# Kernel optimization log

Hardware: AMD Instinct MI355X
Metric: run time of the kernel (lower is better)

Reference implementation:

```python
import jax, jax.numpy as jnp
import numpy as np

EMBED = 1024
HEADS = 16
DIM_HEAD = EMBED // HEADS
N, L = 4, 2048


def setup_inputs() -> dict:
    key = jax.random.key(0)
    ks = jax.random.split(key, 12)
    s = 0.02
    return {
        "q": jax.random.normal(ks[0], (N, L, EMBED), jnp.float32),
        "k": jax.random.normal(ks[1], (N, L, EMBED), jnp.float32),
        "v": jax.random.normal(ks[2], (N, L, EMBED), jnp.float32),
        "padding_mask": jnp.ones((N, L), dtype=bool),
        "sequence_mask": jnp.zeros((L, L), dtype=bool),
        # Linear(in, out): store weight as [out, in] like torch, bias [out]
        "Wq": jax.random.normal(ks[3], (EMBED, EMBED), jnp.float32) * s,
        "bq": jnp.zeros((EMBED,), jnp.float32),
        "Wk": jax.random.normal(ks[4], (EMBED, EMBED), jnp.float32) * s,
        "bk": jnp.zeros((EMBED,), jnp.float32),
        "Wv": jax.random.normal(ks[5], (EMBED, EMBED), jnp.float32) * s,
        "bv": jnp.zeros((EMBED,), jnp.float32),
        "Wo": jax.random.normal(ks[6], (EMBED, EMBED), jnp.float32) * s,
        "bo": jnp.zeros((EMBED,), jnp.float32),
    }


def reference(q, k, v, padding_mask, sequence_mask, Wq, bq, Wk, bk, Wv, bv, Wo, bo):
    n, lq, _ = q.shape
    lk = k.shape[1]
    # input projections
    qp = (q @ Wq.T + bq).reshape(n, lq, HEADS, DIM_HEAD)
    kp = (k @ Wk.T + bk).reshape(n, lk, HEADS, DIM_HEAD)
    vp = (v @ Wv.T + bv).reshape(n, lk, HEADS, DIM_HEAD)
    # energy: [n, h, lq, lk]
    energy = jnp.einsum('nqhd,nkhd->nhqk', qp, kp)
    attention = jax.nn.softmax(energy / jnp.sqrt(jnp.float32(EMBED)), axis=3)
    # NOTE: the original torch code calls masked_fill (non in-place) and
    # discards the result, so padding_mask / sequence_mask have NO effect.
    # Dropout is also never applied in forward. Replicated faithfully.
    out = jnp.einsum('nhqk,nkhd->nqhd', attention, vp)
    out = out.reshape(n, lq, EMBED)
    return out @ Wo.T + bo
```

## Files before the change

### kernel.cpp

```cpp
#include <hip/hip_runtime.h>
#include <stdint.h>

typedef _Float16 f16;
typedef _Float16 f16x8 __attribute__((ext_vector_type(8)));
typedef _Float16 f16x4 __attribute__((ext_vector_type(4)));
typedef _Float16 f16x2 __attribute__((ext_vector_type(2)));
typedef float f32x4 __attribute__((ext_vector_type(4)));

__device__ __forceinline__ f32x4 mfma16(f16x8 a, f16x8 b, f32x4 c) {
    return __builtin_amdgcn_mfma_f32_16x16x32_f16(a, b, c, 0, 0, 0);
}

__device__ __forceinline__ void gload16(const f16* g, f16* l) {
    __builtin_amdgcn_global_load_lds(
        (const __attribute__((address_space(1))) uint32_t*)g,
        (__attribute__((address_space(3))) uint32_t*)l, 16, 0, 0);
}

__device__ __forceinline__ f16x8 cvt8(f32x4 a, f32x4 b) {
    f16x8 h;
    h[0] = (f16)a[0]; h[1] = (f16)a[1]; h[2] = (f16)a[2]; h[3] = (f16)a[3];
    h[4] = (f16)b[0]; h[5] = (f16)b[1]; h[6] = (f16)b[2]; h[7] = (f16)b[3];
    return h;
}

template <bool A16, bool OUT16>
__device__ __forceinline__ void gemm_fused(const void* __restrict__ Av,
                                           const float* __restrict__ B,
                                           const float* __restrict__ bias,
                                           void* __restrict__ Cout, long ldo,
                                           int biasrow, float scale,
                                           long m0, long n0, f16* As, f16* Bs) {
    int tid = threadIdx.x;
    int lane = tid & 63, w = tid >> 6;
    int wm = w & 1, wn = w >> 1;
    int l15 = lane & 15, quad = lane >> 4;

    int r4 = lane >> 2;
    int g = lane & 3;
    int sc = g ^ ((r4 >> 1) & 3);
    int c4 = (lane & 3) ^ ((lane >> 3) & 3);

    const f16* a16 = (const f16*)Av;
    const float* a32 = (const float*)Av;

    const f16* a16src[2];
    const float* a32src[2];
    const float* b32src[2];
    int lwoff[2];
#pragma unroll
    for (int t = 0; t < 2; ++t) {
        long row = t * 64 + w * 16 + r4;
        if constexpr (A16)
            a16src[t] = a16 + (m0 + row) * 1024 + c4 * 8;
        else
            a32src[t] = a32 + (m0 + row) * 1024 + g * 8;
        b32src[t] = B + (n0 + row) * 1024 + g * 8;
        lwoff[t] = t * 2048 + w * 512;
    }
    int wroff = r4 * 32 + sc * 8;

    f32x4 acc[4][4] = {};

#pragma unroll
    for (int t = 0; t < 2; ++t) {
        if constexpr (A16) {
            gload16(a16src[t], As + lwoff[t]);
        } else {
            f32x4 x0 = *(const f32x4*)(a32src[t]);
            f32x4 x1 = *(const f32x4*)(a32src[t] + 4);
            *(f16x8*)&As[lwoff[t] + wroff] = cvt8(x0, x1);
        }
        f32x4 y0 = *(const f32x4*)(b32src[t]);
        f32x4 y1 = *(const f32x4*)(b32src[t] + 4);
        *(f16x8*)&Bs[lwoff[t] + wroff] = cvt8(y0, y1);
    }
    if constexpr (A16) asm volatile("s_waitcnt vmcnt(0)" ::: "memory");
    asm volatile("s_waitcnt lgkmcnt(0)" ::: "memory");
    __builtin_amdgcn_s_barrier();
    __builtin_amdgcn_sched_barrier(0);

    for (int kt = 0; kt < 32; ++kt) {
        int cur = kt & 1;
        int nxt = cur ^ 1;
        f32x4 la[2][2], lb[2][2];
        if (kt < 31) {
            long ko = (long)(kt + 1) * 32;
#pragma unroll
            for (int t = 0; t < 2; ++t) {
                if constexpr (A16) {
                    gload16(a16src[t] + ko, As + nxt * 4096 + lwoff[t]);
                } else {
                    la[t][0] = *(const f32x4*)(a32src[t] + ko);
                    la[t][1] = *(const f32x4*)(a32src[t] + ko + 4);
                }
                lb[t][0] = *(const f32x4*)(b32src[t] + ko);
                lb[t][1] = *(const f32x4*)(b32src[t] + ko + 4);
            }
        }
        const f16* as = As + cur * 4096;
        const f16* bs = Bs + cur * 4096;
        int cs = (quad ^ ((l15 >> 1) & 3)) * 8;
        f16x8 af[4], bf[4];
#pragma unroll
        for (int t = 0; t < 4; ++t) {
            af[t] = *(const f16x8*)&as[(wm * 64 + t * 16 + l15) * 32 + cs];
            bf[t] = *(const f16x8*)&bs[(wn * 64 + t * 16 + l15) * 32 + cs];
        }
        __builtin_amdgcn_s_setprio(1);
#pragma unroll
        for (int i = 0; i < 4; ++i)
#pragma unroll
            for (int j = 0; j < 4; ++j)
                acc[i][j] = mfma16(af[i], bf[j], acc[i][j]);
        __builtin_amdgcn_s_setprio(0);
        if (kt < 31) {
#pragma unroll
            for (int t = 0; t < 2; ++t) {
                if constexpr (!A16)
                    *(f16x8*)&As[nxt * 4096 + lwoff[t] + wroff] =
                        cvt8(la[t][0], la[t][1]);
                *(f16x8*)&Bs[nxt * 4096 + lwoff[t] + wroff] =
                    cvt8(lb[t][0], lb[t][1]);
            }
            if constexpr (A16) asm volatile("s_waitcnt vmcnt(0)" ::: "memory");
            asm volatile("s_waitcnt lgkmcnt(0)" ::: "memory");
            __builtin_amdgcn_s_barrier();
            __builtin_amdgcn_sched_barrier(0);
        }
    }

#pragma unroll
    for (int i = 0; i < 4; ++i) {
        int mrow = wm * 64 + i * 16 + quad * 4;
#pragma unroll
        for (int j = 0; j < 4; ++j) {
            int ncol = wn * 64 + j * 16 + l15;
            long gn = n0 + ncol;
#pragma unroll
            for (int r = 0; r < 4; ++r) {
                long gm = m0 + mrow + r;
                float v = (acc[i][j][r] + (biasrow ? bias[gm] : bias[gn])) * scale;
                if constexpr (OUT16)
                    ((f16*)Cout)[gm * ldo + gn] = (f16)v;
                else
                    ((float*)Cout)[gm * ldo + gn] = v;
            }
        }
    }
}

__global__ __launch_bounds__(256, 2) void qkv_proj(
    const float* __restrict__ q, const float* __restrict__ k,
    const float* __restrict__ v, const float* __restrict__ Wq,
    const float* __restrict__ Wk, const float* __restrict__ Wv,
    const float* __restrict__ bq, const float* __restrict__ bk,
    const float* __restrict__ bv, f16* __restrict__ Qp, f16* __restrict__ Kp,
    f16* __restrict__ Vt) {
    __shared__ __align__(16) f16 As[2 * 4096];
    __shared__ __align__(16) f16 Bs[2 * 4096];
    int z = blockIdx.z;
    const float* A;
    const float* B;
    const float* bias;
    f16* C;
    long ldo;
    int biasrow;
    float scale;
    if (z == 0) {
        A = q; B = Wq; bias = bq; C = Qp; ldo = 1024; biasrow = 0;
        scale = 0.0450842200277786f;
    } else if (z == 1) {
        A = k; B = Wk; bias = bk; C = Kp; ldo = 1024; biasrow = 0;
        scale = 1.0f;
    } else {
        A = Wv; B = v; bias = bv; C = Vt; ldo = 8192; biasrow = 1;
        scale = 1.0f;
    }
    long m0 = (long)(z == 2 ? blockIdx.y : blockIdx.x) * 128;
    long n0 = (long)(z == 2 ? blockIdx.x : blockIdx.y) * 128;
    gemm_fused<false, true>(A, B, bias, C, ldo, biasrow, scale, m0, n0, As, Bs);
}

__global__ __launch_bounds__(256, 2) void o_proj(const f16* __restrict__ Op,
                                                 const float* __restrict__ Wo,
                                                 const float* __restrict__ bo,
                                                 float* __restrict__ out) {
    __shared__ __align__(16) f16 As[2 * 4096];
    __shared__ __align__(16) f16 Bs[2 * 4096];
    gemm_fused<true, false>(Op, Wo, bo, out, 1024, 0, 1.0f,
                            (long)blockIdx.x * 128, (long)blockIdx.y * 128,
                            As, Bs);
}

__global__ __launch_bounds__(256, 2) void attn256(const f16* __restrict__ Qp,
                                                  const f16* __restrict__ Kp,
                                                  const f16* __restrict__ Vt,
                                                  f16* __restrict__ Op) {
    __shared__ __align__(16) f16 Ps0[128 * 64];
    __shared__ __align__(16) f16 Ps1[128 * 64];
    __shared__ __align__(16) f16 Ks[3][64 * 64];
    __shared__ __align__(16) f16 Vs[3][64 * 64];

    int tid = threadIdx.x;
    int lane = tid & 63, w = tid >> 6;
    int l15 = lane & 15, quad = lane >> 4;
    int b = blockIdx.x;
    int xcd = b & 7, slot = b >> 3;
    int nh = xcd * 8 + (slot >> 3);
    int qp = slot & 7;
    int nb = nh >> 4, h = nh & 15;
    long tok0 = (long)nb * 2048;
    long qrow0 = qp * 256;

    int rg = lane >> 3, cg = (lane & 7) ^ rg;

    const f16* qsrc0 = Qp + (tok0 + qrow0) * 1024 + h * 64;
    const f16* qsrc1 = qsrc0 + 128 * 1024;
#pragma unroll
    for (int t = 0; t < 4; ++t) {
        int rb = w * 32 + t * 8;
        gload16(qsrc0 + (rb + rg) * 1024 + cg * 8, &Ps0[rb * 64]);
        gload16(qsrc1 + (rb + rg) * 1024 + cg * 8, &Ps1[rb * 64]);
    }
    const f16* kptr = Kp + (tok0 + w * 16 + rg) * 1024 + h * 64 + cg * 8;
    const f16* vptr = Vt + ((long)h * 64 + w * 16 + rg) * 8192 + tok0 + cg * 8;
    gload16(kptr, &Ks[0][(w * 16) * 64]);
    gload16(kptr + 8 * 1024, &Ks[0][(w * 16 + 8) * 64]);
    gload16(vptr, &Vs[0][(w * 16) * 64]);
    gload16(vptr + (long)8 * 8192, &Vs[0][(w * 16 + 8) * 64]);
    gload16(kptr + 65536, &Ks[1][(w * 16) * 64]);
    gload16(kptr + 65536 + 8 * 1024, &Ks[1][(w * 16 + 8) * 64]);
    gload16(vptr + 64, &Vs[1][(w * 16) * 64]);
    gload16(vptr + 64 + (long)8 * 8192, &Vs[1][(w * 16 + 8) * 64]);
    const f16* kn = kptr + 2 * 65536;
    const f16* vn = vptr + 2 * 64;

    asm volatile("s_waitcnt vmcnt(8)" ::: "memory");
    f16x8 qf0[2][2], qf1[2][2];
#pragma unroll
    for (int ks = 0; ks < 2; ++ks) {
        int cc = (ks * 4 + quad) ^ (l15 & 7);
#pragma unroll
        for (int j = 0; j < 2; ++j) {
            qf0[ks][j] = *(const f16x8*)&Ps0[(w * 32 + j * 16 + l15) * 64 + cc * 8];
            qf1[ks][j] = *(const f16x8*)&Ps1[(w * 32 + j * 16 + l15) * 64 + cc * 8];
        }
    }
    asm volatile("s_waitcnt vmcnt(4)" ::: "memory");
    __builtin_amdgcn_s_barrier();
    __builtin_amdgcn_sched_barrier(0);

    f32x4 oacc0[2][4] = {}, oacc1[2][4] = {};
    float rs0[2] = {0.f, 0.f}, rs1[2] = {0.f, 0.f};
    const f32x4 z4 = {0.f, 0.f, 0.f, 0.f};

    int cur = 0;
    for (int kt = 0; kt < 32; ++kt) {
        f32x4 sacc0[4][2], sacc1[4][2];
        __builtin_amdgcn_s_setprio(1);
#pragma unroll
        for (int ks = 0; ks < 2; ++ks) {
            int cc = (ks * 4 + quad) ^ (l15 & 7);
            f16x8 a[4];
#pragma unroll
            for (int t = 0; t < 4; ++t)
                a[t] = *(const f16x8*)&Ks[cur][(t * 16 + l15) * 64 + cc * 8];
#pragma unroll
            for (int i = 0; i < 4; ++i)
#pragma unroll
                for (int j = 0; j < 2; ++j) {
                    if (ks == 0) {
                        sacc0[i][j] = mfma16(a[i], qf0[0][j], z4);
                        sacc1[i][j] = mfma16(a[i], qf1[0][j], z4);
                    } else {
                        sacc0[i][j] = mfma16(a[i], qf0[1][j], sacc0[i][j]);
                        sacc1[i][j] = mfma16(a[i], qf1[1][j], sacc1[i][j]);
                    }
                }
        }
        __builtin_amdgcn_s_setprio(0);
        if (kt < 30) {
            int nxt = (cur == 0) ? 2 : cur - 1;
            f16* kd = &Ks[nxt][(w * 16) * 64];
            f16* vd = &Vs[nxt][(w * 16) * 64];
            gload16(kn, kd);
            gload16(kn + 8 * 1024, kd + 8 * 64);
            gload16(vn, vd);
            gload16(vn + (long)8 * 8192, vd + 8 * 64);
            kn += 65536;
            vn += 64;
        }
#pragma unroll
        for (int i = 0; i < 4; ++i) {
#pragma unroll
            for (int j = 0; j < 2; ++j) {
                int qrow = w * 32 + j * 16 + l15;
                int kl = i * 16 + quad * 4;
                int c = kl >> 3;
                int off = qrow * 64 + ((c ^ (qrow & 7)) << 3) + (kl & 7);
                {
                    float p0 = __builtin_amdgcn_exp2f(sacc0[i][j][0]);
                    float p1 = __builtin_amdgcn_exp2f(sacc0[i][j][1]);
                    float p2 = __builtin_amdgcn_exp2f(sacc0[i][j][2]);
                    float p3 = __builtin_amdgcn_exp2f(sacc0[i][j][3]);
                    rs0[j] += (p0 + p1) + (p2 + p3);
                    f16x2 lo = __builtin_bit_cast(f16x2, __builtin_amdgcn_cvt_pkrtz(p0, p1));
                    f16x2 hi = __builtin_bit_cast(f16x2, __builtin_amdgcn_cvt_pkrtz(p2, p3));
                    f16x4 ph;
                    ph[0] = lo[0]; ph[1] = lo[1]; ph[2] = hi[0]; ph[3] = hi[1];
                    *(f16x4*)&Ps0[off] = ph;
                }
                {
                    float p0 = __builtin_amdgcn_exp2f(sacc1[i][j][0]);
                    float p1 = __builtin_amdgcn_exp2f(sacc1[i][j][1]);
                    float p2 = __builtin_amdgcn_exp2f(sacc1[i][j][2]);
                    float p3 = __builtin_amdgcn_exp2f(sacc1[i][j][3]);
                    rs1[j] += (p0 + p1) + (p2 + p3);
                    f16x2 lo = __builtin_bit_cast(f16x2, __builtin_amdgcn_cvt_pkrtz(p0, p1));
                    f16x2 hi = __builtin_bit_cast(f16x2, __builtin_amdgcn_cvt_pkrtz(p2, p3));
                    f16x4 ph;
                    ph[0] = lo[0]; ph[1] = lo[1]; ph[2] = hi[0]; ph[3] = hi[1];
                    *(f16x4*)&Ps1[off] = ph;
                }
            }
        }
        __builtin_amdgcn_s_setprio(1);
#pragma unroll
        for (int ks = 0; ks < 2; ++ks) {
            int cc = (ks * 4 + quad) ^ (l15 & 7);
            f16x8 bf[4];
#pragma unroll
            for (int j = 0; j < 4; ++j)
                bf[j] = *(const f16x8*)&Vs[cur][(j * 16 + l15) * 64 + cc * 8];
            f16x8 af0[2], af1[2];
#pragma unroll
            for (int i = 0; i < 2; ++i) {
                af0[i] = *(const f16x8*)&Ps0[(w * 32 + i * 16 + l15) * 64 + cc * 8];
                af1[i] = *(const f16x8*)&Ps1[(w * 32 + i * 16 + l15) * 64 + cc * 8];
            }
#pragma unroll
            for (int i = 0; i < 2; ++i)
#pragma unroll
                for (int j = 0; j < 4; ++j) {
                    oacc0[i][j] = mfma16(af0[i], bf[j], oacc0[i][j]);
                    oacc1[i][j] = mfma16(af1[i], bf[j], oacc1[i][j]);
                }
        }
        __builtin_amdgcn_s_setprio(0);
        if (kt < 31) {
            if (kt < 30)
                asm volatile("s_waitcnt vmcnt(4)" ::: "memory");
            else
                asm volatile("s_waitcnt vmcnt(0)" ::: "memory");
            __builtin_amdgcn_s_barrier();
            __builtin_amdgcn_sched_barrier(0);
        }
        cur = (cur == 2) ? 0 : cur + 1;
    }

    float* lsi = (float*)&Ks[0][0];
#pragma unroll
    for (int j = 0; j < 2; ++j) {
        rs0[j] += __shfl_xor(rs0[j], 16, 64);
        rs0[j] += __shfl_xor(rs0[j], 32, 64);
        rs1[j] += __shfl_xor(rs1[j], 16, 64);
        rs1[j] += __shfl_xor(rs1[j], 32, 64);
    }
    if (lane < 16) {
        lsi[w * 32 + lane] = 1.0f / rs0[0];
        lsi[w * 32 + 16 + lane] = 1.0f / rs0[1];
        lsi[128 + w * 32 + lane] = 1.0f / rs1[0];
        lsi[128 + w * 32 + 16 + lane] = 1.0f / rs1[1];
    }

    long otok = tok0 + qrow0;
#pragma unroll
    for (int i = 0; i < 2; ++i) {
        int qrow = w * 32 + i * 16 + quad * 4;
#pragma unroll
        for (int j = 0; j < 4; ++j) {
            int d = j * 16 + l15;
#pragma unroll
            for (int r = 0; r < 4; ++r) {
                Op[(otok + qrow + r) * 1024 + h * 64 + d] =
                    (f16)(oacc0[i][j][r] * lsi[qrow + r]);
                Op[(otok + 128 + qrow + r) * 1024 + h * 64 + d] =
                    (f16)(oacc1[i][j][r] * lsi[128 + qrow + r]);
            }
        }
    }
}

extern "C" void kernel_launch(void* const* d_in, const int* in_sizes, int n_in,
                              void* d_out, int out_size, void* d_ws, size_t ws_size,
                              hipStream_t stream) {
    const float* q  = (const float*)d_in[0];
    const float* k  = (const float*)d_in[1];
    const float* v  = (const float*)d_in[2];
    const float* Wq = (const float*)d_in[5];
    const float* bq = (const float*)d_in[6];
    const float* Wk = (const float*)d_in[7];
    const float* bk = (const float*)d_in[8];
    const float* Wv = (const float*)d_in[9];
    const float* bv = (const float*)d_in[10];
    const float* Wo = (const float*)d_in[11];
    const float* bo = (const float*)d_in[12];

    char* ws = (char*)d_ws;
    f16* Qp = (f16*)ws;
    f16* Kp = (f16*)(ws + (16L << 20));
    f16* Vt = (f16*)(ws + (32L << 20));
    f16* Op = (f16*)(ws + (48L << 20));

    qkv_proj<<<dim3(64, 8, 3), 256, 0, stream>>>(q, k, v, Wq, Wk, Wv,
                                                 bq, bk, bv, Qp, Kp, Vt);

    attn256<<<512, 256, 0, stream>>>(Qp, Kp, Vt, Op);

    o_proj<<<dim3(64, 8), 256, 0, stream>>>(Op, Wo, bo, (float*)d_out);
}
```

Baseline: 358.8 us.

## Deepen projection GEMM pipeline to three LDS stages with XCD-aware block mapping

Rewrites the shared projection GEMM as a three-stage LDS pipeline. The activation operand is prefetched into registers three k-tiles ahead, while the weight operand is staged one tile ahead. The async global_load_lds path for the fp16 A operand is replaced with register loads plus LDS stores. Block indices are remapped so that all blocks on one XCD share the same weight column tile, aiming for better L2 reuse. The costs are more LDS (48KB per block), higher register pressure from the in-flight prefetch buffers, and a possible loss of occupancy at two blocks per CU.

```diff
diff --git a/kernel.cpp b/kernel.cpp
--- a/kernel.cpp
+++ b/kernel.cpp
@@ -24,111 +24,142 @@
     return h;
 }
 
-template <bool A16, bool OUT16>
-__device__ __forceinline__ void gemm_fused(const void* __restrict__ Av,
-                                           const float* __restrict__ B,
-                                           const float* __restrict__ bias,
-                                           void* __restrict__ Cout, long ldo,
-                                           int biasrow, float scale,
-                                           long m0, long n0, f16* As, f16* Bs) {
+template <bool DEEP16, bool OUT16>
+__device__ __forceinline__ void gemm_fused(
+    const void* __restrict__ Dmat, const float* __restrict__ Smat,
+    long d0, long s0, bool deepA, const float* __restrict__ bias,
+    void* __restrict__ Cout, long ldo, int biasrow, float scale,
+    long m0, long n0, f16* As, f16* Bs) {
     int tid = threadIdx.x;
     int lane = tid & 63, w = tid >> 6;
     int wm = w & 1, wn = w >> 1;
     int l15 = lane & 15, quad = lane >> 4;
-
     int r4 = lane >> 2;
     int g = lane & 3;
     int sc = g ^ ((r4 >> 1) & 3);
-    int c4 = (lane & 3) ^ ((lane >> 3) & 3);
-
-    const f16* a16 = (const f16*)Av;
-    const float* a32 = (const float*)Av;
-
-    const f16* a16src[2];
-    const float* a32src[2];
-    const float* b32src[2];
-    int lwoff[2];
+    int cs = (quad ^ ((l15 >> 1) & 3)) * 8;
+
+    const f16* d16src[2];
+    const float* d32src[2];
+    const float* ssrc[2];
+    int lw[2];
 #pragma unroll
     for (int t = 0; t < 2; ++t) {
         long row = t * 64 + w * 16 + r4;
-        if constexpr (A16)
-            a16src[t] = a16 + (m0 + row) * 1024 + c4 * 8;
+        if constexpr (DEEP16)
+            d16src[t] = (const f16*)Dmat + (d0 + row) * 1024 + g * 8;
         else
-            a32src[t] = a32 + (m0 + row) * 1024 + g * 8;
-        b32src[t] = B + (n0 + row) * 1024 + g * 8;
-        lwoff[t] = t * 2048 + w * 512;
-    }
-    int wroff = r4 * 32 + sc * 8;
-
+            d32src[t] = (const float*)Dmat + (d0 + row) * 1024 + g * 8;
+        ssrc[t] = Smat + (s0 + row) * 1024 + g * 8;
+        lw[t] = t * 2048 + w * 512 + r4 * 32 + sc * 8;
+    }
+    f16* Dlds = deepA ? As : Bs;
+    f16* Slds = deepA ? Bs : As;
+
+    f32x4 dd[3][2][2];
+    f16x8 dh[3][2];
     f32x4 acc[4][4] = {};
 
-#pragma unroll
-    for (int t = 0; t < 2; ++t) {
-        if constexpr (A16) {
-            gload16(a16src[t], As + lwoff[t]);
-        } else {
-            f32x4 x0 = *(const f32x4*)(a32src[t]);
-            f32x4 x1 = *(const f32x4*)(a32src[t] + 4);
-            *(f16x8*)&As[lwoff[t] + wroff] = cvt8(x0, x1);
-        }
-        f32x4 y0 = *(const f32x4*)(b32src[t]);
-        f32x4 y1 = *(const f32x4*)(b32src[t] + 4);
-        *(f16x8*)&Bs[lwoff[t] + wroff] = cvt8(y0, y1);
-    }
-    if constexpr (A16) asm volatile("s_waitcnt vmcnt(0)" ::: "memory");
-    asm volatile("s_waitcnt lgkmcnt(0)" ::: "memory");
-    __builtin_amdgcn_s_barrier();
-    __builtin_amdgcn_sched_barrier(0);
-
-    for (int kt = 0; kt < 32; ++kt) {
-        int cur = kt & 1;
-        int nxt = cur ^ 1;
-        f32x4 la[2][2], lb[2][2];
-        if (kt < 31) {
-            long ko = (long)(kt + 1) * 32;
-#pragma unroll
-            for (int t = 0; t < 2; ++t) {
-                if constexpr (A16) {
-                    gload16(a16src[t] + ko, As + nxt * 4096 + lwoff[t]);
-                } else {
-                    la[t][0] = *(const f32x4*)(a32src[t] + ko);
-                    la[t][1] = *(const f32x4*)(a32src[t] + ko + 4);
-                }
-                lb[t][0] = *(const f32x4*)(b32src[t] + ko);
-                lb[t][1] = *(const f32x4*)(b32src[t] + ko + 4);
-            }
-        }
-        const f16* as = As + cur * 4096;
-        const f16* bs = Bs + cur * 4096;
-        int cs = (quad ^ ((l15 >> 1) & 3)) * 8;
-        f16x8 af[4], bf[4];
-#pragma unroll
-        for (int t = 0; t < 4; ++t) {
-            af[t] = *(const f16x8*)&as[(wm * 64 + t * 16 + l15) * 32 + cs];
-            bf[t] = *(const f16x8*)&bs[(wn * 64 + t * 16 + l15) * 32 + cs];
-        }
-        __builtin_amdgcn_s_setprio(1);
-#pragma unroll
-        for (int i = 0; i < 4; ++i)
-#pragma unroll
-            for (int j = 0; j < 4; ++j)
-                acc[i][j] = mfma16(af[i], bf[j], acc[i][j]);
-        __builtin_amdgcn_s_setprio(0);
-        if (kt < 31) {
-#pragma unroll
-            for (int t = 0; t < 2; ++t) {
-                if constexpr (!A16)
-                    *(f16x8*)&As[nxt * 4096 + lwoff[t] + wroff] =
-                        cvt8(la[t][0], la[t][1]);
-                *(f16x8*)&Bs[nxt * 4096 + lwoff[t] + wroff] =
-                    cvt8(lb[t][0], lb[t][1]);
-            }
-            if constexpr (A16) asm volatile("s_waitcnt vmcnt(0)" ::: "memory");
-            asm volatile("s_waitcnt lgkmcnt(0)" ::: "memory");
-            __builtin_amdgcn_s_barrier();
-            __builtin_amdgcn_sched_barrier(0);
-        }
-    }
+#define ISSUE_D(SET, KO)                                                      \
+    do {                                                                      \
+        _Pragma("unroll") for (int t_ = 0; t_ < 2; ++t_) {                    \
+            if constexpr (DEEP16) {                                           \
+                dh[SET][t_] = *(const f16x8*)(d16src[t_] + (KO));             \
+            } else {                                                          \
+                dd[SET][t_][0] = *(const f32x4*)(d32src[t_] + (KO));          \
+                dd[SET][t_][1] = *(const f32x4*)(d32src[t_] + (KO) + 4);      \
+            }                                                                 \
+        }                                                                     \
+    } while (0)
+
+#define COMMIT_D(SET, SLOT)                                                   \
+    do {                                                                      \
+        _Pragma("unroll") for (int t_ = 0; t_ < 2; ++t_) {                    \
+            if constexpr (DEEP16)                                             \
+                *(f16x8*)&Dlds[(SLOT) * 4096 + lw[t_]] = dh[SET][t_];         \
+            else                                                              \
+                *(f16x8*)&Dlds[(SLOT) * 4096 + lw[t_]] =                      \
+                    cvt8(dd[SET][t_][0], dd[SET][t_][1]);                     \
+        }                                                                     \
+    } while (0)
+
+#define STAGE_S(KO)                                                           \
+    do {                                                                      \
+        _Pragma("unroll") for (int t_ = 0; t_ < 2; ++t_) {                    \
+            ls[t_][0] = *(const f32x4*)(ssrc[t_] + (KO));                     \
+            ls[t_][1] = *(const f32x4*)(ssrc[t_] + (KO) + 4);                 \
+        }                                                                     \
+    } while (0)
+
+#define COMMIT_S(SLOT)                                                        \
+    do {                                                                      \
+        _Pragma("unroll") for (int t_ = 0; t_ < 2; ++t_)                      \
+            *(f16x8*)&Slds[(SLOT) * 4096 + lw[t_]] =                          \
+                cvt8(ls[t_][0], ls[t_][1]);                                   \
+    } while (0)
+
+#define COMPUTE(SLOT)                                                         \
+    do {                                                                      \
+        const f16* as_ = As + (SLOT) * 4096;                                  \
+        const f16* bs_ = Bs + (SLOT) * 4096;                                  \
+        f16x8 af[4], bf[4];                                                   \
+        _Pragma("unroll") for (int t_ = 0; t_ < 4; ++t_) {                    \
+            af[t_] = *(const f16x8*)&as_[(wm * 64 + t_ * 16 + l15) * 32 + cs];\
+            bf[t_] = *(const f16x8*)&bs_[(wn * 64 + t_ * 16 + l15) * 32 + cs];\
+        }                                                                     \
+        __builtin_amdgcn_s_setprio(1);                                        \
+        _Pragma("unroll") for (int i_ = 0; i_ < 4; ++i_)                      \
+            _Pragma("unroll") for (int j_ = 0; j_ < 4; ++j_)                  \
+                acc[i_][j_] = mfma16(af[i_], bf[j_], acc[i_][j_]);            \
+        __builtin_amdgcn_s_setprio(0);                                        \
+    } while (0)
+
+#define SYNC()                                                                \
+    do {                                                                      \
+        asm volatile("s_waitcnt lgkmcnt(0)" ::: "memory");                    \
+        __builtin_amdgcn_s_barrier();                                         \
+        __builtin_amdgcn_sched_barrier(0);                                    \
+    } while (0)
+
+#define GBODY(KT, SI, SC, SLC, SLW)                                           \
+    do {                                                                      \
+        f32x4 ls[2][2];                                                       \
+        if ((KT) <= 28) ISSUE_D(SI, (long)((KT) + 3) * 32);                   \
+        if ((KT) <= 30) STAGE_S((long)((KT) + 1) * 32);                       \
+        COMPUTE(SLC);                                                         \
+        if ((KT) <= 30) {                                                     \
+            COMMIT_D(SC, SLW);                                                \
+            COMMIT_S(SLW);                                                    \
+            SYNC();                                                           \
+        }                                                                     \
+    } while (0)
+
+    ISSUE_D(0, 0);
+    {
+        f32x4 ls[2][2];
+        STAGE_S(0);
+        COMMIT_D(0, 0);
+        COMMIT_S(0);
+    }
+    ISSUE_D(1, 32);
+    ISSUE_D(2, 64);
+    SYNC();
+
+    for (int kt = 0; kt < 30; kt += 3) {
+        GBODY(kt, 0, 1, 0, 1);
+        GBODY(kt + 1, 1, 2, 1, 2);
+        GBODY(kt + 2, 2, 0, 2, 0);
+    }
+    GBODY(30, 0, 1, 0, 1);
+    GBODY(31, 1, 2, 1, 2);
+
+#undef ISSUE_D
+#undef COMMIT_D
+#undef STAGE_S
+#undef COMMIT_S
+#undef COMPUTE
+#undef SYNC
+#undef GBODY
 
 #pragma unroll
     for (int i = 0; i < 4; ++i) {
@@ -157,40 +188,57 @@
     const float* __restrict__ bq, const float* __restrict__ bk,
     const float* __restrict__ bv, f16* __restrict__ Qp, f16* __restrict__ Kp,
     f16* __restrict__ Vt) {
-    __shared__ __align__(16) f16 As[2 * 4096];
-    __shared__ __align__(16) f16 Bs[2 * 4096];
-    int z = blockIdx.z;
-    const float* A;
-    const float* B;
+    __shared__ __align__(16) f16 As[3 * 4096];
+    __shared__ __align__(16) f16 Bs[3 * 4096];
+    int lin = blockIdx.x + (blockIdx.y << 6) + (blockIdx.z << 9);
+    int xcd = lin & 7;
+    int s = lin >> 3;
+    int z = s >> 6;
+    int xi = s & 63;
+    int yi = xcd;
+
+    const float* D;
+    const float* S;
     const float* bias;
     f16* C;
     long ldo;
     int biasrow;
     float scale;
-    if (z == 0) {
-        A = q; B = Wq; bias = bq; C = Qp; ldo = 1024; biasrow = 0;
-        scale = 0.0450842200277786f;
-    } else if (z == 1) {
-        A = k; B = Wk; bias = bk; C = Kp; ldo = 1024; biasrow = 0;
-        scale = 1.0f;
+    long m0, n0, d0, s0;
+    bool deepA;
+    if (z == 2) {
+        m0 = (long)yi * 128;
+        n0 = (long)xi * 128;
+        D = v; d0 = n0; S = Wv; s0 = m0; deepA = false;
+        bias = bv; C = Vt; ldo = 8192; biasrow = 1; scale = 1.0f;
     } else {
-        A = Wv; B = v; bias = bv; C = Vt; ldo = 8192; biasrow = 1;
-        scale = 1.0f;
-    }
-    long m0 = (long)(z == 2 ? blockIdx.y : blockIdx.x) * 128;
-    long n0 = (long)(z == 2 ? blockIdx.x : blockIdx.y) * 128;
-    gemm_fused<false, true>(A, B, bias, C, ldo, biasrow, scale, m0, n0, As, Bs);
+        m0 = (long)xi * 128;
+        n0 = (long)yi * 128;
+        D = (z == 0) ? q : k; d0 = m0;
+        S = (z == 0) ? Wq : Wk; s0 = n0;
+        deepA = true;
+        bias = (z == 0) ? bq : bk;
+        C = (z == 0) ? Qp : Kp;
+        ldo = 1024; biasrow = 0;
+        scale = (z == 0) ? 0.0450842200277786f : 1.0f;
+    }
+    gemm_fused<false, true>(D, S, d0, s0, deepA, bias, C, ldo, biasrow,
+                            scale, m0, n0, As, Bs);
 }
 
 __global__ __launch_bounds__(256, 2) void o_proj(const f16* __restrict__ Op,
                                                  const float* __restrict__ Wo,
                                                  const float* __restrict__ bo,
                                                  float* __restrict__ out) {
-    __shared__ __align__(16) f16 As[2 * 4096];
-    __shared__ __align__(16) f16 Bs[2 * 4096];
-    gemm_fused<true, false>(Op, Wo, bo, out, 1024, 0, 1.0f,
-                            (long)blockIdx.x * 128, (long)blockIdx.y * 128,
-                            As, Bs);
+    __shared__ __align__(16) f16 As[3 * 4096];
+    __shared__ __align__(16) f16 Bs[3 * 4096];
+    int lin = blockIdx.x + (blockIdx.y << 6);
+    int xcd = lin & 7;
+    int s = lin >> 3;
+    long m0 = (long)s * 128;
+    long n0 = (long)xcd * 128;
+    gemm_fused<true, false>(Op, Wo, m0, n0, true, bo, out, 1024, 0, 1.0f,
+                            m0, n0, As, Bs);
 }
 
 __global__ __launch_bounds__(256, 2) void attn256(const f16* __restrict__ Qp,
```

Measured after the change: 379.4 us. 1.06x slower.
